# Optimization experiments

Measured on AMD Instinct MI355X. Metric: run time of the kernel, lower is better.

## Reference

```python
import jax, jax.numpy as jnp
import numpy as np

NUM_LEVELS = 16
FEATURES_PER_LEVEL = 2
LOG2_HASHMAP_SIZE = 19
BASE_RES = 16
FINEST_RES = 2048
N_POINTS = 2097152

_growth = np.exp((np.log(FINEST_RES) - np.log(BASE_RES)) / (NUM_LEVELS - 1))
RESOLUTIONS = np.floor(BASE_RES * _growth ** np.arange(NUM_LEVELS)).astype(np.int64)  # (L,)
TABLE_SIZES = np.minimum(RESOLUTIONS ** 3, 2 ** LOG2_HASHMAP_SIZE).astype(np.int32)   # (L,)
MAX_TABLE_SIZE = 2 ** LOG2_HASHMAP_SIZE

P1, P2, P3 = 73856093, 19349663, 83492791  # spatial hash primes


def setup_inputs() -> dict:
    key = jax.random.key(0)
    k1, k2 = jax.random.split(key)
    coordinates = jax.random.uniform(k1, (N_POINTS, 3), dtype=jnp.float32)
    # keras 'uniform' initializer = U(-0.05, 0.05); tables stacked & zero-padded to max size
    hash_tables = jax.random.uniform(
        k2, (NUM_LEVELS, MAX_TABLE_SIZE, FEATURES_PER_LEVEL),
        minval=-0.05, maxval=0.05, dtype=jnp.float32)
    return {"coordinates": coordinates, "hash_tables": hash_tables}


def reference(coordinates, hash_tables):
    batch_shape = coordinates.shape[:-1]
    coords = coordinates.reshape(-1, 3)  # (N, 3)
    res = jnp.asarray(RESOLUTIONS.astype(np.float32))          # (L,)
    sizes = jnp.asarray(TABLE_SIZES)                            # (L,) int32
    # all levels at once: (L, N, 3)
    grid = jnp.floor(coords[None, :, :] * res[:, None, None]).astype(jnp.int32)
    x, y, t = grid[..., 0], grid[..., 1], grid[..., 2]
    h = (x * np.int32(P1)) ^ (y * np.int32(P2)) ^ (t * np.int32(P3))  # int32 wraparound, like TF
    idx = jnp.abs(h) % sizes[:, None]                           # (L, N)
    feats = jnp.take_along_axis(hash_tables, idx[:, :, None], axis=1)  # (L, N, F)
    out = jnp.transpose(feats, (1, 0, 2)).reshape(coords.shape[0], NUM_LEVELS * FEATURES_PER_LEVEL)
    return out.reshape(*batch_shape, NUM_LEVELS * FEATURES_PER_LEVEL)
```

## Files before the change

### kernel.cpp

```cpp
#include <hip/hip_runtime.h>
#include <stdint.h>


#define TPB 256

typedef float vfloat4 __attribute__((ext_vector_type(4)));
typedef float vfloat2 __attribute__((ext_vector_type(2)));

__device__ __forceinline__ uint32_t hash_idx(float cx, float cy, float cz,
                                             int resi, int siz)
{
    const float rf = (float)resi;
    const int x = (int)floorf(cx * rf);
    const int y = (int)floorf(cy * rf);
    const int z = (int)floorf(cz * rf);
    const uint32_t h = (uint32_t)x * 73856093u
                     ^ (uint32_t)y * 19349663u
                     ^ (uint32_t)z * 83492791u;
    const int32_t hs = (int32_t)h;
    if (siz == (1 << 19)) {
        const uint32_t a = (hs < 0) ? (0u - h) : h;
        return a & 0x7FFFFu;
    } else {
        int32_t a = (hs < 0) ? (int32_t)(0u - h) : hs;
        int32_t r = a % siz;
        if (r < 0) r += siz;
        return (uint32_t)r;
    }
}

#define RESI_LIST {16, 22, 30, 42, 58, 80, 111, 153, \
                   212, 294, 406, 561, 776, 1072, 1482, 2048}
#define SIZ_LIST  {4096, 10648, 27000, 74088, 195112, 512000, \
                   524288, 524288, 524288, 524288, 524288, \
                   524288, 524288, 524288, 524288, 524288}

template<int L0, int L1>
__global__ __launch_bounds__(TPB) void hashenc_gather_lv(
    const float* __restrict__ coords,
    const float* __restrict__ tables,
    float2* __restrict__ ws,
    int npts)
{
    constexpr int RESI[16] = RESI_LIST;
    constexpr int SIZ[16] = SIZ_LIST;

    const int t = threadIdx.x;
    const long long base = (long long)blockIdx.x * 1024;

    float cx[4], cy[4], cz[4];
#pragma unroll
    for (int j = 0; j < 4; ++j) {
        const long long p = base + j * 256 + t;
        cx[j] = coords[3 * p + 0];
        cy[j] = coords[3 * p + 1];
        cz[j] = coords[3 * p + 2];
    }

#pragma unroll
    for (int l = L0; l < L1; ++l) {
        const float* tab = tables + ((size_t)l << 20);
        vfloat2 g[4];
#pragma unroll
        for (int j = 0; j < 4; ++j) {
            const uint32_t idx = hash_idx(cx[j], cy[j], cz[j], RESI[l], SIZ[l]);
            g[j] = *reinterpret_cast<const vfloat2*>(tab + ((size_t)idx << 1));
        }
        float2* wl = ws + (size_t)l * npts + base;
#pragma unroll
        for (int j = 0; j < 4; ++j)
            __builtin_nontemporal_store(g[j],
                reinterpret_cast<vfloat2*>(wl + j * 256 + t));
    }
}

__global__ __launch_bounds__(TPB) void hashenc_transpose(
    const float2* __restrict__ ws,
    float* __restrict__ out,
    int npts)
{
    __shared__ float buf[128 * 33];

    const int t = threadIdx.x;
    const long long pbase = (long long)blockIdx.x * TPB;
    const long long p = pbase + t;

    vfloat2 feat[16];
#pragma unroll
    for (int l = 0; l < 16; ++l)
        feat[l] = __builtin_nontemporal_load(
            reinterpret_cast<const vfloat2*>(ws + (size_t)l * npts + p));

    float* oblk = out + pbase * 32;
#pragma unroll
    for (int h = 0; h < 2; ++h) {
        if ((t >> 7) == h) {
            const int r = t & 127;
#pragma unroll
            for (int l = 0; l < 16; ++l) {
                buf[r * 33 + 2 * l + 0] = feat[l].x;
                buf[r * 33 + 2 * l + 1] = feat[l].y;
            }
        }
        __syncthreads();
#pragma unroll
        for (int k = 0; k < 4; ++k) {
            const int f = k * 1024 + t * 4;
            const int row = f >> 5;
            const int col = f & 31;
            const vfloat4 v = *reinterpret_cast<const vfloat4*>(&buf[row * 33 + col]);
            __builtin_nontemporal_store(v,
                reinterpret_cast<vfloat4*>(&oblk[(long long)h * 4096 + f]));
        }
        __syncthreads();
    }
}

__global__ __launch_bounds__(TPB) void hashenc_kernel(
    const float* __restrict__ coords,
    const float* __restrict__ tables,
    float* __restrict__ out,
    int npts)
{
    constexpr int RESI[16] = RESI_LIST;
    constexpr int SIZ[16] = SIZ_LIST;

    __shared__ float buf[128 * 33];

    const int t = threadIdx.x;
    const long long pbase = (long long)blockIdx.x * TPB;
    const long long p = pbase + t;

    const float cx = coords[3 * p + 0];
    const float cy = coords[3 * p + 1];
    const float cz = coords[3 * p + 2];

    float2 feat[16];
#pragma unroll
    for (int l = 0; l < 16; ++l) {
        const uint32_t idx = hash_idx(cx, cy, cz, RESI[l], SIZ[l]);
        feat[l] = *reinterpret_cast<const float2*>(
            tables + ((size_t)l << 20) + ((size_t)idx << 1));
    }

    float* oblk = out + pbase * 32;
#pragma unroll
    for (int h = 0; h < 2; ++h) {
        if ((t >> 7) == h) {
            const int r = t & 127;
#pragma unroll
            for (int l = 0; l < 16; ++l) {
                buf[r * 33 + 2 * l + 0] = feat[l].x;
                buf[r * 33 + 2 * l + 1] = feat[l].y;
            }
        }
        __syncthreads();
#pragma unroll
        for (int k = 0; k < 4; ++k) {
            const int f = k * 1024 + t * 4;
            const int row = f >> 5;
            const int col = f & 31;
            const vfloat4 v = *reinterpret_cast<const vfloat4*>(&buf[row * 33 + col]);
            __builtin_nontemporal_store(v,
                reinterpret_cast<vfloat4*>(&oblk[(long long)h * 4096 + f]));
        }
        __syncthreads();
    }
}

extern "C" void kernel_launch(void* const* d_in, const int* in_sizes, int n_in,
                              void* d_out, int out_size, void* d_ws, size_t ws_size,
                              hipStream_t stream)
{
    const float* coords = (const float*)d_in[0];
    const float* tables = (const float*)d_in[1];
    float* out = (float*)d_out;
    const int npts = in_sizes[0] / 3;

    const size_t need = (size_t)16 * (size_t)npts * sizeof(float2);
    if (ws_size >= need && (npts % 1024) == 0) {
        float2* ws = (float2*)d_ws;
        const dim3 g(npts / 1024), b(TPB);
        hipLaunchKernelGGL((hashenc_gather_lv<0, 5>),   g, b, 0, stream, coords, tables, ws, npts);
        hipLaunchKernelGGL((hashenc_gather_lv<5, 6>),   g, b, 0, stream, coords, tables, ws, npts);
        hipLaunchKernelGGL((hashenc_gather_lv<6, 7>),   g, b, 0, stream, coords, tables, ws, npts);
        hipLaunchKernelGGL((hashenc_gather_lv<7, 8>),   g, b, 0, stream, coords, tables, ws, npts);
        hipLaunchKernelGGL((hashenc_gather_lv<8, 9>),   g, b, 0, stream, coords, tables, ws, npts);
        hipLaunchKernelGGL((hashenc_gather_lv<9, 10>),  g, b, 0, stream, coords, tables, ws, npts);
        hipLaunchKernelGGL((hashenc_gather_lv<10, 11>), g, b, 0, stream, coords, tables, ws, npts);
        hipLaunchKernelGGL((hashenc_gather_lv<11, 12>), g, b, 0, stream, coords, tables, ws, npts);
        hipLaunchKernelGGL((hashenc_gather_lv<12, 13>), g, b, 0, stream, coords, tables, ws, npts);
        hipLaunchKernelGGL((hashenc_gather_lv<13, 14>), g, b, 0, stream, coords, tables, ws, npts);
        hipLaunchKernelGGL((hashenc_gather_lv<14, 15>), g, b, 0, stream, coords, tables, ws, npts);
        hipLaunchKernelGGL((hashenc_gather_lv<15, 16>), g, b, 0, stream, coords, tables, ws, npts);
        hipLaunchKernelGGL(hashenc_transpose, dim3(npts / TPB), b, 0, stream,
                           (const float2*)d_ws, out, npts);
    } else {
        hipLaunchKernelGGL(hashenc_kernel, dim3(npts / TPB), dim3(TPB), 0, stream,
                           coords, tables, out, npts);
    }
}
```

Measured before the change: 338.0 us.

## Fuse small-level gathers into transpose kernel and double points per gather block

The first five levels, whose tables are small enough to stay cache-resident, are now gathered directly inside the final transpose kernel instead of being written to and re-read from the workspace. This drops one launch and five levels of workspace traffic, and shrinks the workspace to 11 levels. Each per-level gather kernel now handles 2048 points per block with 8 loads in flight per thread and reads coordinates inline rather than caching them across levels. The transpose kernel gains hash arithmetic and random small-table loads, which may raise its latency.

After: 327.0 us. 3.3% less time.

```diff
diff --git a/kernel.cpp b/kernel.cpp
--- a/kernel.cpp
+++ b/kernel.cpp
@@ -35,7 +35,7 @@
                    524288, 524288, 524288, 524288, 524288, \
                    524288, 524288, 524288, 524288, 524288}
 
-template<int L0, int L1>
+template<int LV>
 __global__ __launch_bounds__(TPB) void hashenc_gather_lv(
     const float* __restrict__ coords,
     const float* __restrict__ tables,
@@ -46,50 +46,57 @@
     constexpr int SIZ[16] = SIZ_LIST;
 
     const int t = threadIdx.x;
-    const long long base = (long long)blockIdx.x * 1024;
-
-    float cx[4], cy[4], cz[4];
-#pragma unroll
-    for (int j = 0; j < 4; ++j) {
+    const long long base = (long long)blockIdx.x * 2048;
+    const float* tab = tables + ((size_t)LV << 20);
+
+    vfloat2 g[8];
+#pragma unroll
+    for (int j = 0; j < 8; ++j) {
         const long long p = base + j * 256 + t;
-        cx[j] = coords[3 * p + 0];
-        cy[j] = coords[3 * p + 1];
-        cz[j] = coords[3 * p + 2];
-    }
-
-#pragma unroll
-    for (int l = L0; l < L1; ++l) {
-        const float* tab = tables + ((size_t)l << 20);
-        vfloat2 g[4];
-#pragma unroll
-        for (int j = 0; j < 4; ++j) {
-            const uint32_t idx = hash_idx(cx[j], cy[j], cz[j], RESI[l], SIZ[l]);
-            g[j] = *reinterpret_cast<const vfloat2*>(tab + ((size_t)idx << 1));
-        }
-        float2* wl = ws + (size_t)l * npts + base;
-#pragma unroll
-        for (int j = 0; j < 4; ++j)
-            __builtin_nontemporal_store(g[j],
-                reinterpret_cast<vfloat2*>(wl + j * 256 + t));
-    }
-}
-
-__global__ __launch_bounds__(TPB) void hashenc_transpose(
+        const float cx = coords[3 * p + 0];
+        const float cy = coords[3 * p + 1];
+        const float cz = coords[3 * p + 2];
+        const uint32_t idx = hash_idx(cx, cy, cz, RESI[LV], SIZ[LV]);
+        g[j] = *reinterpret_cast<const vfloat2*>(tab + ((size_t)idx << 1));
+    }
+    float2* wl = ws + (size_t)(LV - 5) * npts + base;
+#pragma unroll
+    for (int j = 0; j < 8; ++j)
+        __builtin_nontemporal_store(g[j],
+            reinterpret_cast<vfloat2*>(wl + j * 256 + t));
+}
+
+__global__ __launch_bounds__(TPB) void hashenc_transpose_fused(
+    const float* __restrict__ coords,
+    const float* __restrict__ tables,
     const float2* __restrict__ ws,
     float* __restrict__ out,
     int npts)
 {
+    constexpr int RESI[16] = RESI_LIST;
+    constexpr int SIZ[16] = SIZ_LIST;
+
     __shared__ float buf[128 * 33];
 
     const int t = threadIdx.x;
     const long long pbase = (long long)blockIdx.x * TPB;
     const long long p = pbase + t;
 
+    const float cx = coords[3 * p + 0];
+    const float cy = coords[3 * p + 1];
+    const float cz = coords[3 * p + 2];
+
     vfloat2 feat[16];
 #pragma unroll
-    for (int l = 0; l < 16; ++l)
+    for (int l = 0; l < 5; ++l) {
+        const uint32_t idx = hash_idx(cx, cy, cz, RESI[l], SIZ[l]);
+        feat[l] = *reinterpret_cast<const vfloat2*>(
+            tables + ((size_t)l << 20) + ((size_t)idx << 1));
+    }
+#pragma unroll
+    for (int l = 5; l < 16; ++l)
         feat[l] = __builtin_nontemporal_load(
-            reinterpret_cast<const vfloat2*>(ws + (size_t)l * npts + p));
+            reinterpret_cast<const vfloat2*>(ws + (size_t)(l - 5) * npts + p));
 
     float* oblk = out + pbase * 32;
 #pragma unroll
@@ -177,24 +184,23 @@
     float* out = (float*)d_out;
     const int npts = in_sizes[0] / 3;
 
-    const size_t need = (size_t)16 * (size_t)npts * sizeof(float2);
-    if (ws_size >= need && (npts % 1024) == 0) {
+    const size_t need = (size_t)11 * (size_t)npts * sizeof(float2);
+    if (ws_size >= need && (npts % 2048) == 0) {
         float2* ws = (float2*)d_ws;
-        const dim3 g(npts / 1024), b(TPB);
-        hipLaunchKernelGGL((hashenc_gather_lv<0, 5>),   g, b, 0, stream, coords, tables, ws, npts);
-        hipLaunchKernelGGL((hashenc_gather_lv<5, 6>),   g, b, 0, stream, coords, tables, ws, npts);
-        hipLaunchKernelGGL((hashenc_gather_lv<6, 7>),   g, b, 0, stream, coords, tables, ws, npts);
-        hipLaunchKernelGGL((hashenc_gather_lv<7, 8>),   g, b, 0, stream, coords, tables, ws, npts);
-        hipLaunchKernelGGL((hashenc_gather_lv<8, 9>),   g, b, 0, stream, coords, tables, ws, npts);
-        hipLaunchKernelGGL((hashenc_gather_lv<9, 10>),  g, b, 0, stream, coords, tables, ws, npts);
-        hipLaunchKernelGGL((hashenc_gather_lv<10, 11>), g, b, 0, stream, coords, tables, ws, npts);
-        hipLaunchKernelGGL((hashenc_gather_lv<11, 12>), g, b, 0, stream, coords, tables, ws, npts);
-        hipLaunchKernelGGL((hashenc_gather_lv<12, 13>), g, b, 0, stream, coords, tables, ws, npts);
-        hipLaunchKernelGGL((hashenc_gather_lv<13, 14>), g, b, 0, stream, coords, tables, ws, npts);
-        hipLaunchKernelGGL((hashenc_gather_lv<14, 15>), g, b, 0, stream, coords, tables, ws, npts);
-        hipLaunchKernelGGL((hashenc_gather_lv<15, 16>), g, b, 0, stream, coords, tables, ws, npts);
-        hipLaunchKernelGGL(hashenc_transpose, dim3(npts / TPB), b, 0, stream,
-                           (const float2*)d_ws, out, npts);
+        const dim3 g(npts / 2048), b(TPB);
+        hipLaunchKernelGGL((hashenc_gather_lv<5>),  g, b, 0, stream, coords, tables, ws, npts);
+        hipLaunchKernelGGL((hashenc_gather_lv<6>),  g, b, 0, stream, coords, tables, ws, npts);
+        hipLaunchKernelGGL((hashenc_gather_lv<7>),  g, b, 0, stream, coords, tables, ws, npts);
+        hipLaunchKernelGGL((hashenc_gather_lv<8>),  g, b, 0, stream, coords, tables, ws, npts);
+        hipLaunchKernelGGL((hashenc_gather_lv<9>),  g, b, 0, stream, coords, tables, ws, npts);
+        hipLaunchKernelGGL((hashenc_gather_lv<10>), g, b, 0, stream, coords, tables, ws, npts);
+        hipLaunchKernelGGL((hashenc_gather_lv<11>), g, b, 0, stream, coords, tables, ws, npts);
+        hipLaunchKernelGGL((hashenc_gather_lv<12>), g, b, 0, stream, coords, tables, ws, npts);
+        hipLaunchKernelGGL((hashenc_gather_lv<13>), g, b, 0, stream, coords, tables, ws, npts);
+        hipLaunchKernelGGL((hashenc_gather_lv<14>), g, b, 0, stream, coords, tables, ws, npts);
+        hipLaunchKernelGGL((hashenc_gather_lv<15>), g, b, 0, stream, coords, tables, ws, npts);
+        hipLaunchKernelGGL(hashenc_transpose_fused, dim3(npts / TPB), b, 0, stream,
+                           coords, tables, (const float2*)d_ws, out, npts);
     } else {
         hipLaunchKernelGGL(hashenc_kernel, dim3(npts / TPB), dim3(TPB), 0, stream,
                            coords, tables, out, npts);
```
